# Kernel optimization log

Measured on AMD Instinct MI355X. Metric: run time of the kernel, lower is better.

The kernel has to match this reference:

```python
import jax, jax.numpy as jnp
import numpy as np

N_HEADS = 16
HEAD_DIM = 64
ATTN_WINDOW = 128
ROPE_BASE = 10000.0


def _rotate_half(x):
    # (x0, x1) -> (-x1, x0) over interleaved pairs in the last dim
    xr = x.reshape(*x.shape[:-1], -1, 2)
    out = jnp.stack((-xr[..., 1], xr[..., 0]), axis=-1)
    return out.reshape(x.shape)


def _rope_cos_sin(T, rotary_dim, base, dtype):
    inv_freq = 1.0 / (base ** (jnp.arange(0, rotary_dim, 2, dtype=jnp.float32) / rotary_dim))
    t = jnp.arange(T, dtype=jnp.float32)
    freqs = t[:, None] * inv_freq[None, :]            # (T, rotary_dim/2)
    cos = jnp.repeat(jnp.cos(freqs), 2, axis=-1)      # (T, rotary_dim)
    sin = jnp.repeat(jnp.sin(freqs), 2, axis=-1)
    return cos.astype(dtype), sin.astype(dtype)


def _apply_rope(x, cos, sin):
    # x: (B, H, T, Dh); rotary_dim == Dh here (rope_fraction = 1.0)
    c = cos[None, None, :, :]
    s = sin[None, None, :, :]
    return x * c + _rotate_half(x) * s


def setup_inputs() -> dict:
    key = jax.random.key(0)
    ks = jax.random.split(key, 5)
    B, T, C = 2, 2048, 1024
    x = jax.random.normal(ks[0], (B, T, C), dtype=jnp.float32)
    Wqkv = jax.random.normal(ks[1], (C, 3 * C), dtype=jnp.float32) * 0.02
    bqkv = jax.random.normal(ks[2], (3 * C,), dtype=jnp.float32) * 0.02
    Wproj = jax.random.normal(ks[3], (C, C), dtype=jnp.float32) * 0.02
    bproj = jax.random.normal(ks[4], (C,), dtype=jnp.float32) * 0.02
    return {"x": x, "Wqkv": Wqkv, "bqkv": bqkv, "Wproj": Wproj, "bproj": bproj}


def reference(x, Wqkv, bqkv, Wproj, bproj):
    B, T, C = x.shape
    H, Dh = N_HEADS, HEAD_DIM

    qkv = x @ Wqkv + bqkv                              # (B, T, 3C)
    q, k, v = jnp.split(qkv, 3, axis=-1)

    def heads(t):
        return t.reshape(B, T, H, Dh).transpose(0, 2, 1, 3)  # (B, H, T, Dh)
    q, k, v = heads(q), heads(k), heads(v)

    cos, sin = _rope_cos_sin(T, Dh, ROPE_BASE, x.dtype)
    q = _apply_rope(q, cos, sin)
    k = _apply_rope(k, cos, sin)

    # local causal mask: allowed iff 0 <= i - j < attn_window
    idx = jnp.arange(T)
    rel = idx[:, None] - idx[None, :]
    allowed = (rel >= 0) & (rel < ATTN_WINDOW)         # (T, T)

    scale = 1.0 / jnp.sqrt(jnp.asarray(Dh, dtype=x.dtype))
    scores = jnp.einsum("bhqd,bhkd->bhqk", q, k) * scale
    scores = jnp.where(allowed[None, None], scores, jnp.asarray(-jnp.inf, dtype=x.dtype))
    attn = jax.nn.softmax(scores, axis=-1)
    attn_out = jnp.einsum("bhqk,bhkd->bhqd", attn, v)  # (B, H, T, Dh)

    attn_out = attn_out.transpose(0, 2, 1, 3).reshape(B, T, C)
    return attn_out @ Wproj + bproj
```

## Files before the change

kernel.cpp:

```cpp
#include <hip/hip_runtime.h>


using bf16x8 = short  __attribute__((ext_vector_type(8)));
using f32x4  = float __attribute__((ext_vector_type(4)));

__device__ __forceinline__ float bf2f(unsigned short u) {
    return __uint_as_float(((unsigned int)u) << 16);
}
__device__ __forceinline__ unsigned short f2bf(float f) {
    unsigned int u = __float_as_uint(f);
    u += 0x7fffu + ((u >> 16) & 1u);
    return (unsigned short)(u >> 16);
}

__device__ __forceinline__ void gload_lds16(const unsigned short* g,
                                            unsigned short* l) {
    __builtin_amdgcn_global_load_lds(
        (const __attribute__((address_space(1))) unsigned int*)(g),
        (__attribute__((address_space(3))) unsigned int*)(l),
        16, 0, 0);
}

__global__ __launch_bounds__(256) void f32_to_bf16_kernel(
        const float* __restrict__ in, unsigned short* __restrict__ out, int n4) {
    int i = blockIdx.x * 256 + threadIdx.x;
    int stride = gridDim.x * 256;
    for (; i < n4; i += stride) {
        float4 v = ((const float4*)in)[i];
        ushort4 o;
        o.x = f2bf(v.x); o.y = f2bf(v.y); o.z = f2bf(v.z); o.w = f2bf(v.w);
        ((ushort4*)out)[i] = o;
    }
}

__global__ __launch_bounds__(256) void transpose_f32_bf16(
        const float* __restrict__ W, unsigned short* __restrict__ WT,
        int rows, int cols) {
    __shared__ unsigned short tile[32][33];
    int c0 = blockIdx.x * 32, r0 = blockIdx.y * 32;
    int tx = threadIdx.x, ty = threadIdx.y;
    for (int i = ty; i < 32; i += 8)
        tile[i][tx] = f2bf(W[(size_t)(r0 + i) * cols + c0 + tx]);
    __syncthreads();
    for (int i = ty; i < 32; i += 8)
        WT[(size_t)(c0 + i) * rows + r0 + tx] = tile[tx][i];
}

template <int BM, int BN, int WM, int WN, bool OUT_BF16, bool FUSE_ROPE>
__global__ __launch_bounds__(256) void gemm_lds(
        const unsigned short* __restrict__ A,
        const unsigned short* __restrict__ Bt,
        const float* __restrict__ bias,
        void* __restrict__ Cv,
        const float* __restrict__ tab,
        int M, int N, int K) {
    constexpr int MI = BM / 16;
    constexpr int NI = BN / 16;
    constexpr int PW = (MI + NI) / 4;
    constexpr int WGN = BN / WN;
    constexpr int MR = WM / 16, NR = WN / 16;

    __shared__ unsigned short As[2][BM * 32];
    __shared__ unsigned short Bs[2][BN * 32];

    int row0 = blockIdx.y * BM, col0 = blockIdx.x * BN;
    int tid = threadIdx.x;
    int lane = tid & 63, wid = tid >> 6;
    int wr = wid / WGN, wc = wid % WGN;
    int fr = lane & 15, kq = lane >> 4;
    int r_in = lane >> 2, cg8 = (lane & 3) * 8;

    f32x4 acc[MR][NR];
    #pragma unroll
    for (int i = 0; i < MR; ++i)
        #pragma unroll
        for (int j = 0; j < NR; ++j)
            acc[i][j] = (f32x4){0.f, 0.f, 0.f, 0.f};

    auto stage = [&](int buf, int kt) {
        #pragma unroll
        for (int t = 0; t < PW; ++t) {
            int j = wid * PW + t;
            if (j < MI) {
                int row = j * 16 + r_in;
                gload_lds16(A + (size_t)(row0 + row) * K + kt + cg8,
                            &As[buf][j * 512]);
            } else {
                int jb = j - MI;
                int row = jb * 16 + r_in;
                gload_lds16(Bt + (size_t)(col0 + row) * K + kt + cg8,
                            &Bs[buf][jb * 512]);
            }
        }
    };
    auto compute = [&](int buf) {
        bf16x8 af[MR], bfv[NR];
        #pragma unroll
        for (int i = 0; i < MR; ++i)
            af[i] = *(const bf16x8*)&As[buf][(wr * WM + i * 16 + fr) * 32 + kq * 8];
        #pragma unroll
        for (int j = 0; j < NR; ++j)
            bfv[j] = *(const bf16x8*)&Bs[buf][(wc * WN + j * 16 + fr) * 32 + kq * 8];
        #pragma unroll
        for (int i = 0; i < MR; ++i)
            #pragma unroll
            for (int j = 0; j < NR; ++j)
                acc[i][j] = __builtin_amdgcn_mfma_f32_16x16x32_bf16(
                                af[i], bfv[j], acc[i][j], 0, 0, 0);
    };

    stage(0, 0);
    __syncthreads();
    int cur = 0;
    for (int kt = 32; kt < K; kt += 32) {
        stage(cur ^ 1, kt);
        compute(cur);
        __syncthreads();
        cur ^= 1;
    }
    compute(cur);

    int rg = kq * 4;
    #pragma unroll
    for (int j = 0; j < NR; ++j) {
        int col = col0 + wc * WN + j * 16 + fr;
        float bz = bias[col];
        #pragma unroll
        for (int i = 0; i < MR; ++i) {
            float v4[4];
            #pragma unroll
            for (int r = 0; r < 4; ++r) v4[r] = acc[i][j][r] + bz;
            if constexpr (FUSE_ROPE) {
                if (col0 < 2048) {
                    int ii = (j * 16 + fr) >> 1;
                    bool odd = fr & 1;
                    #pragma unroll
                    for (int r = 0; r < 4; ++r) {
                        float part = __shfl_xor(v4[r], 1);
                        int t = (row0 + wr * WM + i * 16 + rg + r) & 2047;
                        float c = tab[(t * 32 + ii) * 2];
                        float s = tab[(t * 32 + ii) * 2 + 1];
                        v4[r] = odd ? fmaf(v4[r], c,  part * s)
                                    : fmaf(v4[r], c, -part * s);
                    }
                }
            }
            #pragma unroll
            for (int r = 0; r < 4; ++r) {
                int row = row0 + wr * WM + i * 16 + rg + r;
                if constexpr (OUT_BF16)
                    ((unsigned short*)Cv)[(size_t)row * N + col] = f2bf(v4[r]);
                else
                    ((float*)Cv)[(size_t)row * N + col] = v4[r];
            }
        }
    }
}

__global__ __launch_bounds__(256) void rope_table_kernel(float* __restrict__ tab) {
    int idx = blockIdx.x * 256 + threadIdx.x;
    int t = idx >> 5, i = idx & 31;
    float inv = powf(10000.0f, -(float)i / 32.0f);
    float ang = (float)t * inv;
    tab[idx * 2]     = cosf(ang);
    tab[idx * 2 + 1] = sinf(ang);
}

#define VTS 200
#define PSS 168

__global__ __launch_bounds__(256) void attn_kernel(
        const unsigned short* __restrict__ qkv, unsigned short* __restrict__ aout) {
    __shared__ unsigned short Vt[64 * VTS];
    __shared__ unsigned short Ps[4 * 16 * PSS];

    int bid = blockIdx.x;
    int h  = bid & 15;
    int qt = (bid >> 4) & 31;
    int b  = bid >> 9;
    int Q0 = qt * 64;
    int kbase = Q0 - 127; if (kbase < 0) kbase = 0;
    int nk = Q0 + 64 - kbase;
    int tid = threadIdx.x;

    {
        int r32 = tid & 31;
        int c8  = (tid >> 5) * 8;
        #pragma unroll
        for (int p = 0; p < 7; ++p) {
            int r = p * 32 + r32;
            if (r < VTS) {
                unsigned int wv[4] = {0u, 0u, 0u, 0u};
                if (r < nk) {
                    uint4 v = *(const uint4*)(qkv +
                        (size_t)(b * 2048 + kbase + r) * 3072 + 2048 + h * 64 + c8);
                    wv[0] = v.x; wv[1] = v.y; wv[2] = v.z; wv[3] = v.w;
                }
                #pragma unroll
                for (int j = 0; j < 4; ++j) {
                    Vt[(c8 + 2 * j)     * VTS + r] = (unsigned short)(wv[j] & 0xffffu);
                    Vt[(c8 + 2 * j + 1) * VTS + r] = (unsigned short)(wv[j] >> 16);
                }
            }
        }
    }
    __syncthreads();

    int lane = tid & 63, w = tid >> 6;
    int qw0 = Q0 + w * 16;
    int lo = lane & 15, hi = lane >> 4;

    const unsigned short* qg =
        qkv + (size_t)(b * 2048 + qw0 + lo) * 3072 + h * 64 + hi * 8;
    bf16x8 aq0 = *(const bf16x8*)qg;
    bf16x8 aq1 = *(const bf16x8*)(qg + 32);

    int klo = qw0 - 127; if (klo < kbase) klo = kbase;
    int t0 = (klo - kbase) >> 4;
    int t1 = (qw0 + 15 - kbase) >> 4;
    int ntiles = t1 - t0 + 1;
    if ((ntiles & 1) && t0 > 0) { --t0; ++ntiles; }
    int nks = (ntiles + 1) >> 1;
    int wkb = t0 * 16;

    f32x4 s[10];
    #pragma unroll
    for (int i = 0; i < 10; ++i) s[i] = (f32x4){0.f, 0.f, 0.f, 0.f};
    #pragma unroll
    for (int i = 0; i < 10; ++i) {
        if (i < ntiles) {
            const unsigned short* kg = qkv +
                (size_t)(b * 2048 + kbase + (t0 + i) * 16 + lo) * 3072
                + 1024 + h * 64 + hi * 8;
            bf16x8 bk0 = *(const bf16x8*)kg;
            bf16x8 bk1 = *(const bf16x8*)(kg + 32);
            s[i] = __builtin_amdgcn_mfma_f32_16x16x32_bf16(aq0, bk0, s[i], 0, 0, 0);
            s[i] = __builtin_amdgcn_mfma_f32_16x16x32_bf16(aq1, bk1, s[i], 0, 0, 0);
        }
    }

    const float scale = 0.125f;
    float mx[4] = {-1e30f, -1e30f, -1e30f, -1e30f};
    #pragma unroll
    for (int i = 0; i < 10; ++i) {
        if (i < ntiles) {
            int ka = kbase + (t0 + i) * 16 + lo;
            #pragma unroll
            for (int r = 0; r < 4; ++r) {
                int rel = (qw0 + hi * 4 + r) - ka;
                bool ok = (rel >= 0) && (rel < 128);
                float v = ok ? s[i][r] * scale : -1e30f;
                s[i][r] = v;
                mx[r] = fmaxf(mx[r], v);
            }
        }
    }
    #pragma unroll
    for (int r = 0; r < 4; ++r)
        #pragma unroll
        for (int o = 1; o < 16; o <<= 1)
            mx[r] = fmaxf(mx[r], __shfl_xor(mx[r], o));

    float sum[4] = {0.f, 0.f, 0.f, 0.f};
    #pragma unroll
    for (int i = 0; i < 10; ++i) {
        if (i < ntiles) {
            #pragma unroll
            for (int r = 0; r < 4; ++r) {
                float e = __expf(s[i][r] - mx[r]);
                s[i][r] = e;
                sum[r] += e;
            }
        }
    }
    #pragma unroll
    for (int r = 0; r < 4; ++r) {
        #pragma unroll
        for (int o = 1; o < 16; o <<= 1)
            sum[r] += __shfl_xor(sum[r], o);
        sum[r] = 1.0f / sum[r];
    }

    unsigned short* pw = &Ps[(w * 16) * PSS];
    #pragma unroll
    for (int i = 0; i < 10; ++i) {
        if (i < ntiles) {
            #pragma unroll
            for (int r = 0; r < 4; ++r)
                pw[(hi * 4 + r) * PSS + i * 16 + lo] = f2bf(s[i][r] * sum[r]);
        }
    }
    if (ntiles & 1) {
        int zr = lane >> 2, zc = ntiles * 16 + (lane & 3) * 4;
        *(ushort4*)&pw[zr * PSS + zc] = (ushort4){0, 0, 0, 0};
    }

    f32x4 o[4];
    #pragma unroll
    for (int dt = 0; dt < 4; ++dt) o[dt] = (f32x4){0.f, 0.f, 0.f, 0.f};
    #pragma unroll
    for (int ks = 0; ks < 5; ++ks) {
        if (ks < nks) {
            bf16x8 pa = *(const bf16x8*)&Ps[(w * 16 + lo) * PSS + ks * 32 + hi * 8];
            #pragma unroll
            for (int dt = 0; dt < 4; ++dt) {
                bf16x8 vb = *(const bf16x8*)&Vt[(dt * 16 + lo) * VTS
                                                + wkb + ks * 32 + hi * 8];
                o[dt] = __builtin_amdgcn_mfma_f32_16x16x32_bf16(pa, vb, o[dt], 0, 0, 0);
            }
        }
    }

    #pragma unroll
    for (int dt = 0; dt < 4; ++dt)
        #pragma unroll
        for (int r = 0; r < 4; ++r)
            aout[(size_t)(b * 2048 + qw0 + hi * 4 + r) * 1024
                 + h * 64 + dt * 16 + lo] = f2bf(o[dt][r]);
}

extern "C" void kernel_launch(void* const* d_in, const int* in_sizes, int n_in,
                              void* d_out, int out_size, void* d_ws, size_t ws_size,
                              hipStream_t stream) {
    const float* x     = (const float*)d_in[0];
    const float* Wqkv  = (const float*)d_in[1];
    const float* bqkv  = (const float*)d_in[2];
    const float* Wproj = (const float*)d_in[3];
    const float* bproj = (const float*)d_in[4];
    float* out = (float*)d_out;

    char* ws = (char*)d_ws;
    unsigned short* WqkvT  = (unsigned short*)(ws);
    unsigned short* WprojT = (unsigned short*)(ws + 6291456);
    unsigned short* xb     = (unsigned short*)(ws + 8388608);
    unsigned short* qkv    = (unsigned short*)(ws + 16777216);
    float*          tab    = (float*)        (ws + 41943040);
    unsigned short* attno  = (unsigned short*)(ws + 42467328);

    transpose_f32_bf16<<<dim3(96, 32), dim3(32, 8), 0, stream>>>(Wqkv,  WqkvT,  1024, 3072);
    transpose_f32_bf16<<<dim3(32, 32), dim3(32, 8), 0, stream>>>(Wproj, WprojT, 1024, 1024);
    f32_to_bf16_kernel<<<1024, 256, 0, stream>>>(x, xb, 4194304 / 4);
    rope_table_kernel<<<256, 256, 0, stream>>>(tab);

    gemm_lds<128, 128, 64, 64, true, true>
        <<<dim3(24, 32), 256, 0, stream>>>(xb, WqkvT, bqkv, qkv, tab, 4096, 3072, 1024);
    attn_kernel<<<1024, 256, 0, stream>>>(qkv, attno);
    gemm_lds<128, 64, 32, 64, false, false>
        <<<dim3(16, 32), 256, 0, stream>>>(attno, WprojT, bproj, out, nullptr, 4096, 1024, 1024);
}
```

Measured before the change: 109.4 us.

## Triple-buffer GEMM LDS staging with explicit vmcnt waits and barriers

```diff
diff --git a/kernel.cpp b/kernel.cpp
--- a/kernel.cpp
+++ b/kernel.cpp
@@ -19,6 +19,19 @@
         (const __attribute__((address_space(1))) unsigned int*)(g),
         (__attribute__((address_space(3))) unsigned int*)(l),
         16, 0, 0);
+}
+
+template <int N>
+__device__ __forceinline__ void vm_wait() {
+    static_assert(N == 0 || N == 3 || N == 4 || N == 6 || N == 8, "add case");
+    if constexpr (N == 0)      asm volatile("s_waitcnt vmcnt(0)" ::: "memory");
+    else if constexpr (N == 3) asm volatile("s_waitcnt vmcnt(3)" ::: "memory");
+    else if constexpr (N == 4) asm volatile("s_waitcnt vmcnt(4)" ::: "memory");
+    else if constexpr (N == 6) asm volatile("s_waitcnt vmcnt(6)" ::: "memory");
+    else                       asm volatile("s_waitcnt vmcnt(8)" ::: "memory");
+}
+__device__ __forceinline__ void lgkm_wait0() {
+    asm volatile("s_waitcnt lgkmcnt(0)" ::: "memory");
 }
 
 __global__ __launch_bounds__(256) void f32_to_bf16_kernel(
@@ -60,8 +73,8 @@
     constexpr int WGN = BN / WN;
     constexpr int MR = WM / 16, NR = WN / 16;
 
-    __shared__ unsigned short As[2][BM * 32];
-    __shared__ unsigned short Bs[2][BN * 32];
+    __shared__ unsigned short As[3][BM * 32];
+    __shared__ unsigned short Bs[3][BN * 32];
 
     int row0 = blockIdx.y * BM, col0 = blockIdx.x * BN;
     int tid = threadIdx.x;
@@ -109,16 +122,22 @@
                                 af[i], bfv[j], acc[i][j], 0, 0, 0);
     };
 
+    int nt = K >> 5;
     stage(0, 0);
-    __syncthreads();
-    int cur = 0;
-    for (int kt = 32; kt < K; kt += 32) {
-        stage(cur ^ 1, kt);
-        compute(cur);
-        __syncthreads();
-        cur ^= 1;
-    }
-    compute(cur);
+    stage(1, 32);
+    stage(2, 64);
+    int t = 0;
+    for (; t < nt - 3; ++t) {
+        vm_wait<2 * PW>();
+        __builtin_amdgcn_s_barrier();
+        compute(t % 3);
+        lgkm_wait0();
+        __builtin_amdgcn_s_barrier();
+        stage(t % 3, (t + 3) * 32);
+    }
+    vm_wait<2 * PW>(); __builtin_amdgcn_s_barrier(); compute(t % 3); ++t;
+    vm_wait<PW>();     __builtin_amdgcn_s_barrier(); compute(t % 3); ++t;
+    vm_wait<0>();      __builtin_amdgcn_s_barrier(); compute(t % 3);
 
     int rg = kq * 4;
     #pragma unroll
@@ -137,9 +156,9 @@
                     #pragma unroll
                     for (int r = 0; r < 4; ++r) {
                         float part = __shfl_xor(v4[r], 1);
-                        int t = (row0 + wr * WM + i * 16 + rg + r) & 2047;
-                        float c = tab[(t * 32 + ii) * 2];
-                        float s = tab[(t * 32 + ii) * 2 + 1];
+                        int trow = (row0 + wr * WM + i * 16 + rg + r) & 2047;
+                        float c = tab[(trow * 32 + ii) * 2];
+                        float s = tab[(trow * 32 + ii) * 2 + 1];
                         v4[r] = odd ? fmaf(v4[r], c,  part * s)
                                     : fmaf(v4[r], c, -part * s);
                     }
```

Result: slower. 116.5 us (+6.5%).

## Replace QKV GEMM with 256x256-tile 512-thread kernel using swizzled LDS

Applied to the files above, without the earlier changes.

```diff
diff --git a/kernel.cpp b/kernel.cpp
--- a/kernel.cpp
+++ b/kernel.cpp
@@ -19,6 +19,13 @@
         (const __attribute__((address_space(1))) unsigned int*)(g),
         (__attribute__((address_space(3))) unsigned int*)(l),
         16, 0, 0);
+}
+
+template <int N>
+__device__ __forceinline__ void vm_wait() {
+    static_assert(N == 0 || N == 8, "add case");
+    if constexpr (N == 0) asm volatile("s_waitcnt vmcnt(0)" ::: "memory");
+    else                  asm volatile("s_waitcnt vmcnt(8)" ::: "memory");
 }
 
 __global__ __launch_bounds__(256) void f32_to_bf16_kernel(
@@ -46,13 +53,135 @@
         WT[(size_t)(c0 + i) * rows + r0 + tx] = tile[tx][i];
 }
 
-template <int BM, int BN, int WM, int WN, bool OUT_BF16, bool FUSE_ROPE>
+template <bool FUSE_ROPE>
+__global__ __launch_bounds__(512, 2) void gemm256(
+        const unsigned short* __restrict__ A,
+        const unsigned short* __restrict__ Bt,
+        const float* __restrict__ bias,
+        unsigned short* __restrict__ C,
+        const float* __restrict__ tab,
+        int M, int N, int K) {
+    __shared__ unsigned short Ab[2][256 * 64];
+    __shared__ unsigned short Bb[2][256 * 64];
+
+    int row0 = blockIdx.y * 256, col0 = blockIdx.x * 256;
+    int tid = threadIdx.x;
+    int lane = tid & 63, wid = tid >> 6;
+    int wr = wid >> 2, wc = wid & 3;
+    int fr = lane & 15, kq = lane >> 4;
+
+    int srow_in = lane >> 3;
+    int sp0  = (lane & 7) * 8;
+    int scol = sp0 ^ (srow_in << 3);
+
+    f32x4 acc[8][4];
+    #pragma unroll
+    for (int i = 0; i < 8; ++i)
+        #pragma unroll
+        for (int j = 0; j < 4; ++j) acc[i][j] = (f32x4){0.f, 0.f, 0.f, 0.f};
+
+    auto stage = [&](int buf, int kt) {
+        #pragma unroll
+        for (int g = 0; g < 4; ++g) {
+            int ra = wid * 32 + g * 8;
+            gload_lds16(A + (size_t)(row0 + ra + srow_in) * K + kt + scol,
+                        &Ab[buf][ra * 64]);
+        }
+        #pragma unroll
+        for (int g = 0; g < 4; ++g) {
+            int rb = wid * 32 + g * 8;
+            gload_lds16(Bt + (size_t)(col0 + rb + srow_in) * K + kt + scol,
+                        &Bb[buf][rb * 64]);
+        }
+    };
+
+    int swz = (fr & 7) << 3;
+    auto compute = [&](const unsigned short* Ap, const unsigned short* Bp) {
+        bf16x8 bv[4][2];
+        #pragma unroll
+        for (int j = 0; j < 4; ++j)
+            #pragma unroll
+            for (int kk = 0; kk < 2; ++kk)
+                bv[j][kk] = *(const bf16x8*)&Bp[(wc * 64 + j * 16 + fr) * 64
+                                                + ((kk * 32 + kq * 8) ^ swz)];
+        #pragma unroll
+        for (int q = 0; q < 4; ++q) {
+            bf16x8 av[2][2];
+            #pragma unroll
+            for (int ii = 0; ii < 2; ++ii)
+                #pragma unroll
+                for (int kk = 0; kk < 2; ++kk)
+                    av[ii][kk] = *(const bf16x8*)
+                        &Ap[(wr * 128 + (q * 2 + ii) * 16 + fr) * 64
+                            + ((kk * 32 + kq * 8) ^ swz)];
+            __builtin_amdgcn_s_setprio(1);
+            #pragma unroll
+            for (int ii = 0; ii < 2; ++ii)
+                #pragma unroll
+                for (int kk = 0; kk < 2; ++kk)
+                    #pragma unroll
+                    for (int j = 0; j < 4; ++j)
+                        acc[q * 2 + ii][j] = __builtin_amdgcn_mfma_f32_16x16x32_bf16(
+                            av[ii][kk], bv[j][kk], acc[q * 2 + ii][j], 0, 0, 0);
+            __builtin_amdgcn_s_setprio(0);
+        }
+    };
+
+    int nt = K >> 6;
+    stage(0, 0);
+    for (int t = 0; t < nt; ++t) {
+        int c = t & 1;
+        if (t + 1 < nt) {
+            stage(c ^ 1, (t + 1) << 6);
+            vm_wait<8>();
+        } else {
+            vm_wait<0>();
+        }
+        __builtin_amdgcn_s_barrier();
+        compute(Ab[c], Bb[c]);
+        __builtin_amdgcn_s_barrier();
+    }
+
+    int rg = kq * 4;
+    #pragma unroll
+    for (int j = 0; j < 4; ++j) {
+        int col = col0 + wc * 64 + j * 16 + fr;
+        float bz = bias[col];
+        #pragma unroll
+        for (int i = 0; i < 8; ++i) {
+            float v4[4];
+            #pragma unroll
+            for (int r = 0; r < 4; ++r) v4[r] = acc[i][j][r] + bz;
+            if constexpr (FUSE_ROPE) {
+                if (col0 < 2048) {
+                    int ii2 = (j * 16 + fr) >> 1;
+                    bool odd = fr & 1;
+                    #pragma unroll
+                    for (int r = 0; r < 4; ++r) {
+                        float part = __shfl_xor(v4[r], 1);
+                        int trow = (row0 + wr * 128 + i * 16 + rg + r) & 2047;
+                        float cc = tab[(trow * 32 + ii2) * 2];
+                        float ss = tab[(trow * 32 + ii2) * 2 + 1];
+                        v4[r] = odd ? fmaf(v4[r], cc,  part * ss)
+                                    : fmaf(v4[r], cc, -part * ss);
+                    }
+                }
+            }
+            #pragma unroll
+            for (int r = 0; r < 4; ++r) {
+                int row = row0 + wr * 128 + i * 16 + rg + r;
+                C[(size_t)row * N + col] = f2bf(v4[r]);
+            }
+        }
+    }
+}
+
+template <int BM, int BN, int WM, int WN, bool OUT_BF16>
 __global__ __launch_bounds__(256) void gemm_lds(
         const unsigned short* __restrict__ A,
         const unsigned short* __restrict__ Bt,
         const float* __restrict__ bias,
         void* __restrict__ Cv,
-        const float* __restrict__ tab,
         int M, int N, int K) {
     constexpr int MI = BM / 16;
     constexpr int NI = BN / 16;
@@ -127,31 +256,14 @@
         float bz = bias[col];
         #pragma unroll
         for (int i = 0; i < MR; ++i) {
-            float v4[4];
-            #pragma unroll
-            for (int r = 0; r < 4; ++r) v4[r] = acc[i][j][r] + bz;
-            if constexpr (FUSE_ROPE) {
-                if (col0 < 2048) {
-                    int ii = (j * 16 + fr) >> 1;
-                    bool odd = fr & 1;
-                    #pragma unroll
-                    for (int r = 0; r < 4; ++r) {
-                        float part = __shfl_xor(v4[r], 1);
-                        int t = (row0 + wr * WM + i * 16 + rg + r) & 2047;
-                        float c = tab[(t * 32 + ii) * 2];
-                        float s = tab[(t * 32 + ii) * 2 + 1];
-                        v4[r] = odd ? fmaf(v4[r], c,  part * s)
-                                    : fmaf(v4[r], c, -part * s);
-                    }
-                }
-            }
             #pragma unroll
             for (int r = 0; r < 4; ++r) {
                 int row = row0 + wr * WM + i * 16 + rg + r;
+                float val = acc[i][j][r] + bz;
                 if constexpr (OUT_BF16)
-                    ((unsigned short*)Cv)[(size_t)row * N + col] = f2bf(v4[r]);
+                    ((unsigned short*)Cv)[(size_t)row * N + col] = f2bf(val);
                 else
-                    ((float*)Cv)[(size_t)row * N + col] = v4[r];
+                    ((float*)Cv)[(size_t)row * N + col] = val;
             }
         }
     }
@@ -342,9 +454,9 @@
     f32_to_bf16_kernel<<<1024, 256, 0, stream>>>(x, xb, 4194304 / 4);
     rope_table_kernel<<<256, 256, 0, stream>>>(tab);
 
-    gemm_lds<128, 128, 64, 64, true, true>
-        <<<dim3(24, 32), 256, 0, stream>>>(xb, WqkvT, bqkv, qkv, tab, 4096, 3072, 1024);
+    gemm256<true><<<dim3(12, 16), 512, 0, stream>>>(
+        xb, WqkvT, bqkv, qkv, tab, 4096, 3072, 1024);
     attn_kernel<<<1024, 256, 0, stream>>>(qkv, attno);
-    gemm_lds<128, 64, 32, 64, false, false>
-        <<<dim3(16, 32), 256, 0, stream>>>(attno, WprojT, bproj, out, nullptr, 4096, 1024, 1024);
-}
+    gemm_lds<128, 64, 32, 64, false>
+        <<<dim3(16, 32), 256, 0, stream>>>(attno, WprojT, bproj, out, 4096, 1024, 1024);
+}
```

New measurement: 118.2 us. 1.08x slower.

## Merge prep kernels into one launch and stage QKV GEMM epilogue through LDS

Applied to the files above, without the earlier changes.

```diff
diff --git a/kernel.cpp b/kernel.cpp
--- a/kernel.cpp
+++ b/kernel.cpp
@@ -21,29 +21,40 @@
         16, 0, 0);
 }
 
-__global__ __launch_bounds__(256) void f32_to_bf16_kernel(
-        const float* __restrict__ in, unsigned short* __restrict__ out, int n4) {
-    int i = blockIdx.x * 256 + threadIdx.x;
-    int stride = gridDim.x * 256;
-    for (; i < n4; i += stride) {
-        float4 v = ((const float4*)in)[i];
-        ushort4 o;
-        o.x = f2bf(v.x); o.y = f2bf(v.y); o.z = f2bf(v.z); o.w = f2bf(v.w);
-        ((ushort4*)out)[i] = o;
-    }
-}
-
-__global__ __launch_bounds__(256) void transpose_f32_bf16(
-        const float* __restrict__ W, unsigned short* __restrict__ WT,
-        int rows, int cols) {
+__global__ __launch_bounds__(256) void prep_kernel(
+        const float* __restrict__ Wqkv, const float* __restrict__ Wproj,
+        const float* __restrict__ x,
+        unsigned short* __restrict__ WqkvT, unsigned short* __restrict__ WprojT,
+        unsigned short* __restrict__ xb, float* __restrict__ tab) {
     __shared__ unsigned short tile[32][33];
-    int c0 = blockIdx.x * 32, r0 = blockIdx.y * 32;
-    int tx = threadIdx.x, ty = threadIdx.y;
-    for (int i = ty; i < 32; i += 8)
-        tile[i][tx] = f2bf(W[(size_t)(r0 + i) * cols + c0 + tx]);
-    __syncthreads();
-    for (int i = ty; i < 32; i += 8)
-        WT[(size_t)(c0 + i) * rows + r0 + tx] = tile[tx][i];
+    int blk = blockIdx.x;
+    int tid = threadIdx.x;
+    if (blk < 4096) {
+        const float* W; unsigned short* WT; int cols, bx, by;
+        if (blk < 3072) { W = Wqkv;  WT = WqkvT;  cols = 3072; bx = blk % 96; by = blk / 96; }
+        else            { W = Wproj; WT = WprojT; cols = 1024; bx = (blk - 3072) & 31; by = (blk - 3072) >> 5; }
+        int c0 = bx * 32, r0 = by * 32;
+        int tx = tid & 31, ty = tid >> 5;
+        for (int i = ty; i < 32; i += 8)
+            tile[i][tx] = f2bf(W[(size_t)(r0 + i) * cols + c0 + tx]);
+        __syncthreads();
+        for (int i = ty; i < 32; i += 8)
+            WT[(size_t)(c0 + i) * 1024 + r0 + tx] = tile[tx][i];
+    } else if (blk < 5120) {
+        for (int i = (blk - 4096) * 256 + tid; i < 1048576; i += 262144) {
+            float4 v = ((const float4*)x)[i];
+            ushort4 o;
+            o.x = f2bf(v.x); o.y = f2bf(v.y); o.z = f2bf(v.z); o.w = f2bf(v.w);
+            ((ushort4*)xb)[i] = o;
+        }
+    } else {
+        int idx = (blk - 5120) * 256 + tid;
+        int t = idx >> 5, i = idx & 31;
+        float inv = powf(10000.0f, -(float)i / 32.0f);
+        float ang = (float)t * inv;
+        tab[idx * 2]     = cosf(ang);
+        tab[idx * 2 + 1] = sinf(ang);
+    }
 }
 
 template <int BM, int BN, int WM, int WN, bool OUT_BF16, bool FUSE_ROPE>
@@ -60,8 +71,9 @@
     constexpr int WGN = BN / WN;
     constexpr int MR = WM / 16, NR = WN / 16;
 
-    __shared__ unsigned short As[2][BM * 32];
-    __shared__ unsigned short Bs[2][BN * 32];
+    __shared__ unsigned short smem[2 * (BM + BN) * 32];
+    auto As = [&](int buf) { return &smem[buf * (BM + BN) * 32]; };
+    auto Bs = [&](int buf) { return &smem[buf * (BM + BN) * 32 + BM * 32]; };
 
     int row0 = blockIdx.y * BM, col0 = blockIdx.x * BN;
     int tid = threadIdx.x;
@@ -84,12 +96,12 @@
             if (j < MI) {
                 int row = j * 16 + r_in;
                 gload_lds16(A + (size_t)(row0 + row) * K + kt + cg8,
-                            &As[buf][j * 512]);
+                            As(buf) + j * 512);
             } else {
                 int jb = j - MI;
                 int row = jb * 16 + r_in;
                 gload_lds16(Bt + (size_t)(col0 + row) * K + kt + cg8,
-                            &Bs[buf][jb * 512]);
+                            Bs(buf) + jb * 512);
             }
         }
     };
@@ -97,10 +109,10 @@
         bf16x8 af[MR], bfv[NR];
         #pragma unroll
         for (int i = 0; i < MR; ++i)
-            af[i] = *(const bf16x8*)&As[buf][(wr * WM + i * 16 + fr) * 32 + kq * 8];
+            af[i] = *(const bf16x8*)&As(buf)[(wr * WM + i * 16 + fr) * 32 + kq * 8];
         #pragma unroll
         for (int j = 0; j < NR; ++j)
-            bfv[j] = *(const bf16x8*)&Bs[buf][(wc * WN + j * 16 + fr) * 32 + kq * 8];
+            bfv[j] = *(const bf16x8*)&Bs(buf)[(wc * WN + j * 16 + fr) * 32 + kq * 8];
         #pragma unroll
         for (int i = 0; i < MR; ++i)
             #pragma unroll
@@ -121,49 +133,66 @@
     compute(cur);
 
     int rg = kq * 4;
-    #pragma unroll
-    for (int j = 0; j < NR; ++j) {
-        int col = col0 + wc * WN + j * 16 + fr;
-        float bz = bias[col];
-        #pragma unroll
-        for (int i = 0; i < MR; ++i) {
-            float v4[4];
-            #pragma unroll
-            for (int r = 0; r < 4; ++r) v4[r] = acc[i][j][r] + bz;
-            if constexpr (FUSE_ROPE) {
-                if (col0 < 2048) {
-                    int ii = (j * 16 + fr) >> 1;
-                    bool odd = fr & 1;
-                    #pragma unroll
-                    for (int r = 0; r < 4; ++r) {
-                        float part = __shfl_xor(v4[r], 1);
-                        int t = (row0 + wr * WM + i * 16 + rg + r) & 2047;
-                        float c = tab[(t * 32 + ii) * 2];
-                        float s = tab[(t * 32 + ii) * 2 + 1];
-                        v4[r] = odd ? fmaf(v4[r], c,  part * s)
-                                    : fmaf(v4[r], c, -part * s);
+    if constexpr (OUT_BF16) {
+        static_assert(BM * BN <= 2 * (BM + BN) * 32, "epilogue tile must fit");
+        unsigned short* Ct = smem;
+        __syncthreads();
+        #pragma unroll
+        for (int j = 0; j < NR; ++j) {
+            int colL = wc * WN + j * 16 + fr;
+            float bz = bias[col0 + colL];
+            #pragma unroll
+            for (int i = 0; i < MR; ++i) {
+                float v4[4];
+                #pragma unroll
+                for (int r = 0; r < 4; ++r) v4[r] = acc[i][j][r] + bz;
+                if constexpr (FUSE_ROPE) {
+                    if (col0 < 2048) {
+                        int ii2 = (colL & 63) >> 1;
+                        bool odd = fr & 1;
+                        #pragma unroll
+                        for (int r = 0; r < 4; ++r) {
+                            float part = __shfl_xor(v4[r], 1);
+                            int trow = (row0 + wr * WM + i * 16 + rg + r) & 2047;
+                            float cc = tab[(trow * 32 + ii2) * 2];
+                            float ss = tab[(trow * 32 + ii2) * 2 + 1];
+                            v4[r] = odd ? fmaf(v4[r], cc,  part * ss)
+                                        : fmaf(v4[r], cc, -part * ss);
+                        }
                     }
                 }
-            }
-            #pragma unroll
-            for (int r = 0; r < 4; ++r) {
-                int row = row0 + wr * WM + i * 16 + rg + r;
-                if constexpr (OUT_BF16)
-                    ((unsigned short*)Cv)[(size_t)row * N + col] = f2bf(v4[r]);
-                else
-                    ((float*)Cv)[(size_t)row * N + col] = v4[r];
-            }
-        }
-    }
-}
-
-__global__ __launch_bounds__(256) void rope_table_kernel(float* __restrict__ tab) {
-    int idx = blockIdx.x * 256 + threadIdx.x;
-    int t = idx >> 5, i = idx & 31;
-    float inv = powf(10000.0f, -(float)i / 32.0f);
-    float ang = (float)t * inv;
-    tab[idx * 2]     = cosf(ang);
-    tab[idx * 2 + 1] = sinf(ang);
+                #pragma unroll
+                for (int r = 0; r < 4; ++r)
+                    Ct[(wr * WM + i * 16 + rg + r) * BN + colL] = f2bf(v4[r]);
+            }
+        }
+        __syncthreads();
+        unsigned short* C = (unsigned short*)Cv;
+        int rr = tid >> 4, cc8 = (tid & 15) * (BN / 16);
+        #pragma unroll
+        for (int p = 0; p < BM / 16; ++p) {
+            int row = p * 16 + rr;
+            #pragma unroll
+            for (int q = 0; q < BN / 128; ++q)
+                *(bf16x8*)&C[(size_t)(row0 + row) * N + col0 + cc8 + q * 8] =
+                    *(const bf16x8*)&Ct[row * BN + cc8 + q * 8];
+        }
+    } else {
+        float* C = (float*)Cv;
+        #pragma unroll
+        for (int j = 0; j < NR; ++j) {
+            int col = col0 + wc * WN + j * 16 + fr;
+            float bz = bias[col];
+            #pragma unroll
+            for (int i = 0; i < MR; ++i) {
+                #pragma unroll
+                for (int r = 0; r < 4; ++r) {
+                    int row = row0 + wr * WM + i * 16 + rg + r;
+                    C[(size_t)row * N + col] = acc[i][j][r] + bz;
+                }
+            }
+        }
+    }
 }
 
 #define VTS 200
@@ -337,10 +366,7 @@
     float*          tab    = (float*)        (ws + 41943040);
     unsigned short* attno  = (unsigned short*)(ws + 42467328);
 
-    transpose_f32_bf16<<<dim3(96, 32), dim3(32, 8), 0, stream>>>(Wqkv,  WqkvT,  1024, 3072);
-    transpose_f32_bf16<<<dim3(32, 32), dim3(32, 8), 0, stream>>>(Wproj, WprojT, 1024, 1024);
-    f32_to_bf16_kernel<<<1024, 256, 0, stream>>>(x, xb, 4194304 / 4);
-    rope_table_kernel<<<256, 256, 0, stream>>>(tab);
+    prep_kernel<<<5376, 256, 0, stream>>>(Wqkv, Wproj, x, WqkvT, WprojT, xb, tab);
 
     gemm_lds<128, 128, 64, 64, true, true>
         <<<dim3(24, 32), 256, 0, stream>>>(xb, WqkvT, bqkv, qkv, tab, 4096, 3072, 1024);
```

Result: faster. 103.1 us (-5.8%).
